# Performance work log

Measured on AMD Instinct MI355X. Metric: run time of the kernel, lower is better.

Reference implementation:

```python
import jax, jax.numpy as jnp
import numpy as np


def _block(x, a, b):
    # [..., W, H, D] -> [..., W//a, H//b, a, b, D]
    w, h, d = x.shape[-3:]
    x = jnp.reshape(x, x.shape[:-3] + (w // a, a, h // b, b, d))
    return jnp.moveaxis(x, -4, -3)


def _combine(x, bs):
    # [..., W, H, D] -> [..., W//bs, H//bs, bs*bs*D]
    x = _block(x, bs, bs)
    return jnp.reshape(x, x.shape[:-3] + (-1,))


def _normalize(x):
    x = x - jnp.mean(x, axis=-1, keepdims=True)
    return x / (jnp.linalg.norm(x, axis=-1, keepdims=True) + 1e-05)


def setup_inputs() -> dict:
    key = jax.random.key(0)
    k1, k2 = jax.random.split(key)
    x = jax.random.normal(k1, (8, 128, 128, 64), dtype=jnp.float32)
    y = jax.random.normal(k2, (8, 128, 128, 64), dtype=jnp.float32)
    return {"x": x, "y": y, "blocksize": 4}


def reference(x, y, blocksize):
    shape = x.shape
    xc = _normalize(_combine(x, blocksize))  # [B, W/bs, H/bs, F]
    yc = _normalize(_combine(y, blocksize))
    yf = jnp.reshape(yc, (-1, yc.shape[-1]))  # [M, F] codebook
    # single similarity matrix, reused for min-loss and argmax (original
    # computed jnp.inner twice -- same math)
    sim = jnp.einsum('...f,mf->...m', xc, yf)  # [B, W/bs, H/bs, M]
    cosloss = jnp.mean(jnp.min(1.0 - sim, axis=-1))
    idx = jnp.argmax(sim, axis=-1)
    # one-hot matmul against yf == top-1 gather (argmax picks first max, as
    # does the original I = (argmax - arange == 0) construction)
    new_x = jnp.take(yf, idx, axis=0)  # [B, W/bs, H/bs, F]
    new_x = jnp.reshape(new_x, new_x.shape[:-1] + (blocksize, blocksize, -1))
    new_x = jnp.swapaxes(new_x, -4, -3)
    new_x = jnp.reshape(new_x, shape)
    return cosloss, new_x
```

## Files before the change

### kernel.cpp

```cpp
#include <hip/hip_runtime.h>
#include <math.h>


#define NROWS 8192
#define KY 1024
#define NCH 32
#define EPS 3e-4f
#define FEPS 8e-4f

typedef _Float16 v8h __attribute__((ext_vector_type(8)));
typedef float f32x4 __attribute__((ext_vector_type(4)));

__device__ __forceinline__ void gload16(const _Float16* g, _Float16* l) {
    __builtin_amdgcn_global_load_lds(
        (const __attribute__((address_space(1))) void*)g,
        (__attribute__((address_space(3))) void*)l, 16, 0, 0);
}

__device__ __forceinline__ unsigned umax(unsigned a, unsigned b) { return a > b ? a : b; }
__device__ __forceinline__ unsigned umin(unsigned a, unsigned b) { return a < b ? a : b; }

__device__ __forceinline__ unsigned packKey(float v, int col) {
    unsigned b = __float_as_uint(v);
    b ^= (unsigned)((int)b >> 31) | 0x80000000u;
    return (b & 0xFFFFE000u) | (unsigned)(8191 - col);
}

__device__ __forceinline__ float unpackApprox(unsigned k) {
    unsigned kb = k & 0xFFFFE000u;
    unsigned b = (kb & 0x80000000u) ? (kb ^ 0x80000000u) : ~kb;
    return __uint_as_float(b);
}

#define KMERGE(a1, a2, a3, b1, b2, b3) do {                                 \
    unsigned _n1 = umax(a1, b1);                                            \
    unsigned _n2 = umax(umin(a1, b1), umax(a2, b2));                        \
    unsigned _n3 = umax(umax(a3, b3), umax(umin(a1, b2), umin(a2, b1)));    \
    a1 = _n1; a2 = _n2; a3 = _n3;                                           \
} while (0)

__global__ __launch_bounds__(256) void normSplitKernel(
    const float* __restrict__ x, const float* __restrict__ y,
    _Float16* __restrict__ Xh, _Float16* __restrict__ Xl,
    _Float16* __restrict__ Yh, _Float16* __restrict__ Yl,
    int* __restrict__ flagCnt) {
    if (blockIdx.x == 0 && threadIdx.x == 0) *flagCnt = 0;
    int gr = blockIdx.x * 4 + (threadIdx.x >> 6);
    int ln = threadIdx.x & 63;
    bool isX = gr < NROWS;
    int row = isX ? gr : gr - NROWS;
    const float* src = isX ? x : y;
    _Float16* dh = isX ? Xh : Yh;
    _Float16* dl = isX ? Xl : Yl;
    int b = row >> 10, wq = (row >> 5) & 31, hq = row & 31;
    int a = ln >> 4, c = (ln >> 2) & 3, d0 = (ln & 3) << 4;
    const float* p = &src[(((size_t)(b * 128) + wq * 4 + a) * 128 + hq * 4 + c) * 64 + d0];
    float vv[16];
    *(float4*)(vv + 0)  = *(const float4*)(p + 0);
    *(float4*)(vv + 4)  = *(const float4*)(p + 4);
    *(float4*)(vv + 8)  = *(const float4*)(p + 8);
    *(float4*)(vv + 12) = *(const float4*)(p + 12);
    double s = 0.0;
    #pragma unroll
    for (int q = 0; q < 16; q++) s += (double)vv[q];
    #pragma unroll
    for (int m = 1; m < 64; m <<= 1) s += __shfl_xor(s, m, 64);
    double mean = s * (1.0 / 1024.0);
    double ss = 0.0;
    #pragma unroll
    for (int q = 0; q < 16; q++) {
        double d = (double)vv[q] - mean;
        ss += d * d;
    }
    #pragma unroll
    for (int m = 1; m < 64; m <<= 1) ss += __shfl_xor(ss, m, 64);
    double scale = 1.0 / (sqrt(ss) + 1e-5);
    _Float16 hi[16], lo[16];
    #pragma unroll
    for (int q = 0; q < 16; q++) {
        float f = (float)(((double)vv[q] - mean) * scale);
        _Float16 h = (_Float16)f;
        hi[q] = h;
        lo[q] = (_Float16)(f - (float)h);
    }
    size_t f0 = (size_t)row * KY + (ln << 4);
    *(v8h*)&dh[f0]     = *(v8h*)(hi);
    *(v8h*)&dh[f0 + 8] = *(v8h*)(hi + 8);
    *(v8h*)&dl[f0]     = *(v8h*)(lo);
    *(v8h*)&dl[f0 + 8] = *(v8h*)(lo + 8);
}

__global__ __launch_bounds__(512, 2) void simKernel(
    const _Float16* __restrict__ Xh, const _Float16* __restrict__ Yh,
    float* __restrict__ pV1, unsigned* __restrict__ pK1,
    unsigned* __restrict__ pK2, unsigned* __restrict__ pK3) {
    __shared__ __align__(16) _Float16 As[2][256 * 64];
    __shared__ __align__(16) _Float16 Bs[2][256 * 64];
    __shared__ unsigned sK[2][4][128][3];
    __shared__ float sE[2][4][128];
    const int t = threadIdx.x;
    const int l = t & 63, w = t >> 6;
    const int wr = w >> 2, wc = w & 3;
    const int quad = l >> 4, lm = l & 15;
    const int flat = blockIdx.x;
    const int bx = flat >> 5, by = flat & 31;
    const int r0 = bx * 256, c0 = by * 256;

    f32x4 acc[8][4];
    #pragma unroll
    for (int i = 0; i < 8; i++)
        #pragma unroll
        for (int j = 0; j < 4; j++) acc[i][j] = (f32x4){0.f, 0.f, 0.f, 0.f};

    const int lh = l >> 3, ll = l & 7;
    const int srow = w * 8 + lh;
    const int scol = (ll ^ lh) << 3;
    const _Float16* gA0 = Xh + (size_t)(r0 + srow) * KY + scol;
    const _Float16* gB0 = Yh + (size_t)(c0 + srow) * KY + scol;
    const int ldsS = w * 512;

#define STAGE(bb, kt) do {                                                   \
    const size_t _ko = (size_t)(kt) * 64;                                    \
    gload16(gA0 + _ko,                       &As[bb][ldsS]);                 \
    gload16(gB0 + _ko,                       &Bs[bb][ldsS]);                 \
    gload16(gA0 + (size_t)64  * KY + _ko,    &As[bb][4096 + ldsS]);          \
    gload16(gB0 + (size_t)64  * KY + _ko,    &Bs[bb][4096 + ldsS]);          \
    gload16(gA0 + (size_t)128 * KY + _ko,    &As[bb][8192 + ldsS]);          \
    gload16(gB0 + (size_t)128 * KY + _ko,    &Bs[bb][8192 + ldsS]);          \
    gload16(gA0 + (size_t)192 * KY + _ko,    &As[bb][12288 + ldsS]);         \
    gload16(gB0 + (size_t)192 * KY + _ko,    &Bs[bb][12288 + ldsS]);         \
} while (0)

    const int arow = (wr * 128 + lm) * 64;
    const int brow = (wc * 64 + lm) * 64;
    const int sw7 = lm & 7;

    STAGE(0, 0);
    asm volatile("s_waitcnt vmcnt(0)" ::: "memory");
    __builtin_amdgcn_s_barrier();
    __builtin_amdgcn_sched_barrier(0);

    #pragma unroll 1
    for (int kt = 0; kt < 16; kt++) {
        const int cur = kt & 1;
        STAGE(cur ^ 1, (kt + 1) & 15);
        #pragma unroll
        for (int ks = 0; ks < 2; ks++) {
            const int cA = ((ks * 4 + quad) ^ sw7) << 3;
            v8h af[8], bf[4];
            #pragma unroll
            for (int i = 0; i < 8; i++)
                af[i] = *(const v8h*)&As[cur][arow + i * 1024 + cA];
            #pragma unroll
            for (int j = 0; j < 4; j++)
                bf[j] = *(const v8h*)&Bs[cur][brow + j * 1024 + cA];
            __builtin_amdgcn_s_setprio(1);
            #pragma unroll
            for (int j = 0; j < 4; j++)
                #pragma unroll
                for (int i = 0; i < 8; i++)
                    acc[i][j] = __builtin_amdgcn_mfma_f32_16x16x32_f16(af[i], bf[j], acc[i][j], 0, 0, 0);
            __builtin_amdgcn_s_setprio(0);
        }
        asm volatile("s_waitcnt vmcnt(0)" ::: "memory");
        __builtin_amdgcn_s_barrier();
        __builtin_amdgcn_sched_barrier(0);
    }
#undef STAGE

    const int cbase = c0 + wc * 64 + lm;
    #pragma unroll
    for (int i = 0; i < 8; i++) {
        #pragma unroll
        for (int r = 0; r < 4; r++) {
            float v0 = acc[i][0][r], v1 = acc[i][1][r];
            float v2 = acc[i][2][r], v3 = acc[i][3][r];
            unsigned k0 = packKey(v0, cbase);
            unsigned k1 = packKey(v1, cbase + 16);
            unsigned k2 = packKey(v2, cbase + 32);
            unsigned k3 = packKey(v3, cbase + 48);
            unsigned h1 = umax(k0, k1), l1 = umin(k0, k1);
            unsigned h2 = umax(k2, k3), l2 = umin(k2, k3);
            unsigned a1 = umax(h1, h2);
            unsigned a2 = umax(umin(h1, h2), umax(l1, l2));
            unsigned a3 = umax(umin(h1, l2), umin(l1, h2));
            float ev = fmaxf(fmaxf(v0, v1), fmaxf(v2, v3));
            #pragma unroll
            for (int m = 1; m < 16; m <<= 1) {
                unsigned b1 = (unsigned)__shfl_xor((int)a1, m, 64);
                unsigned b2 = (unsigned)__shfl_xor((int)a2, m, 64);
                unsigned b3 = (unsigned)__shfl_xor((int)a3, m, 64);
                float be = __shfl_xor(ev, m, 64);
                KMERGE(a1, a2, a3, b1, b2, b3);
                ev = fmaxf(ev, be);
            }
            if (lm == 0) {
                int rr = i * 16 + quad * 4 + r;
                sK[wr][wc][rr][0] = a1; sK[wr][wc][rr][1] = a2; sK[wr][wc][rr][2] = a3;
                sE[wr][wc][rr] = ev;
            }
        }
    }
    __syncthreads();
    if (t < 256) {
        const int mwr = t >> 7, ri = t & 127;
        unsigned a1 = sK[mwr][0][ri][0], a2 = sK[mwr][0][ri][1], a3 = sK[mwr][0][ri][2];
        float ev = sE[mwr][0][ri];
        #pragma unroll
        for (int q = 1; q < 4; q++) {
            unsigned b1 = sK[mwr][q][ri][0], b2 = sK[mwr][q][ri][1], b3 = sK[mwr][q][ri][2];
            KMERGE(a1, a2, a3, b1, b2, b3);
            ev = fmaxf(ev, sE[mwr][q][ri]);
        }
        size_t o = (size_t)by * NROWS + (r0 + t);
        pV1[o] = ev;
        pK1[o] = a1; pK2[o] = a2; pK3[o] = a3;
    }
}

__global__ __launch_bounds__(256) void reduceKernel(
    const float* __restrict__ pV1, const unsigned* __restrict__ pK1,
    const unsigned* __restrict__ pK2, const unsigned* __restrict__ pK3,
    int* __restrict__ bestIdx, int* __restrict__ flagRows,
    int* __restrict__ flagC2, int* __restrict__ flagC3,
    int* __restrict__ flagCnt, float* __restrict__ blkSum) {
    int t = threadIdx.x;
    int g = blockIdx.x * 256 + t;
    int row = g >> 2, sub = g & 3;
    unsigned a1 = 0, a2 = 0, a3 = 0;
    float ev = -1e30f;
    #pragma unroll
    for (int k = 0; k < 8; k++) {
        size_t o = (size_t)(sub + (k << 2)) * NROWS + row;
        unsigned b1 = pK1[o], b2 = pK2[o], b3 = pK3[o];
        float e = pV1[o];
        KMERGE(a1, a2, a3, b1, b2, b3);
        ev = fmaxf(ev, e);
    }
    #pragma unroll
    for (int m = 1; m < 4; m <<= 1) {
        unsigned b1 = (unsigned)__shfl_xor((int)a1, m, 64);
        unsigned b2 = (unsigned)__shfl_xor((int)a2, m, 64);
        unsigned b3 = (unsigned)__shfl_xor((int)a3, m, 64);
        float be = __shfl_xor(ev, m, 64);
        KMERGE(a1, a2, a3, b1, b2, b3);
        ev = fmaxf(ev, be);
    }
    bool lead = (t & 3) == 0;
    if (lead) {
        bestIdx[row] = 8191 - (int)(a1 & 8191u);
        if (ev - unpackApprox(a2) < FEPS) {
            int s = atomicAdd(flagCnt, 1);
            flagRows[s] = row;
            flagC2[s] = 8191 - (int)(a2 & 8191u);
            flagC3[s] = 8191 - (int)(a3 & 8191u);
        }
    }
    double sum = lead ? 1.0 - (double)ev : 0.0;
    __shared__ double sh[4];
    #pragma unroll
    for (int off = 32; off; off >>= 1) sum += __shfl_down(sum, off, 64);
    if ((t & 63) == 0) sh[t >> 6] = sum;
    __syncthreads();
    if (t == 0) blkSum[blockIdx.x] = (float)(sh[0] + sh[1] + sh[2] + sh[3]);
}

__global__ __launch_bounds__(256) void refineKernel(
    const _Float16* __restrict__ Xh, const _Float16* __restrict__ Xl,
    const _Float16* __restrict__ Yh, const _Float16* __restrict__ Yl,
    int* __restrict__ bestIdx, const int* __restrict__ flagRows,
    const int* __restrict__ flagC2, const int* __restrict__ flagC3,
    const int* __restrict__ flagCnt) {
    int n = *flagCnt;
    int wave = (blockIdx.x << 2) + (threadIdx.x >> 6);
    int ln = threadIdx.x & 63;
    for (int fi = wave; fi < n; fi += gridDim.x * 4) {
        int row = flagRows[fi];
        int cand[3];
        cand[0] = bestIdx[row]; cand[1] = flagC2[fi]; cand[2] = flagC3[fi];
        double d[3];
        #pragma unroll
        for (int c = 0; c < 3; c++) {
            double p = 0.0;
            int yr = cand[c];
            #pragma unroll
            for (int q = 0; q < 16; q++) {
                int k = (ln << 4) + q;
                float xv = (float)Xh[(size_t)row * KY + k] + (float)Xl[(size_t)row * KY + k];
                float yv = (float)Yh[(size_t)yr * KY + k] + (float)Yl[(size_t)yr * KY + k];
                p += (double)xv * yv;
            }
            #pragma unroll
            for (int m = 1; m < 64; m <<= 1) p += __shfl_xor(p, m, 64);
            d[c] = p;
        }
        if (ln == 0) {
            int bi = cand[0]; double bv = d[0];
            #pragma unroll
            for (int c = 1; c < 3; c++) {
                if (d[c] > bv || (d[c] == bv && cand[c] < bi)) { bv = d[c]; bi = cand[c]; }
            }
            bestIdx[row] = bi;
        }
    }
}

__global__ __launch_bounds__(256) void gatherKernel(
    const _Float16* __restrict__ Yh, const _Float16* __restrict__ Yl,
    const int* __restrict__ bestIdx, const float* __restrict__ blkSum,
    float* __restrict__ out) {
    int t = threadIdx.x;
    if (blockIdx.x == 0 && t == 0) {
        double s = 0.0;
        for (int i = 0; i < 128; i++) s += (double)blkSum[i];
        out[0] = (float)(s / 8192.0);
    }
    int g = (blockIdx.x * 256 + t) << 2;
    int b = g >> 20, wq = (g >> 13) & 127, hq = (g >> 6) & 127, d = g & 63;
    int row = (b << 10) + ((wq >> 2) << 5) + (hq >> 2);
    int f = ((wq & 3) << 8) + ((hq & 3) << 6) + d;
    size_t base = (size_t)bestIdx[row] * KY + f;
    const _Float16* ph = &Yh[base];
    const _Float16* pl = &Yl[base];
    out[1 + g + 0] = (float)ph[0] + (float)pl[0];
    out[1 + g + 1] = (float)ph[1] + (float)pl[1];
    out[1 + g + 2] = (float)ph[2] + (float)pl[2];
    out[1 + g + 3] = (float)ph[3] + (float)pl[3];
}

extern "C" void kernel_launch(void* const* d_in, const int* in_sizes, int n_in,
                              void* d_out, int out_size, void* d_ws, size_t ws_size,
                              hipStream_t stream) {
    const float* x = (const float*)d_in[0];
    const float* y = (const float*)d_in[1];
    float* out = (float*)d_out;
    char* ws = (char*)d_ws;
    _Float16* Xh  = (_Float16*)(ws);
    _Float16* Xl  = (_Float16*)(ws + 16777216u);
    _Float16* Yh  = (_Float16*)(ws + 33554432u);
    _Float16* Yl  = (_Float16*)(ws + 50331648u);
    float* pV1    = (float*)(ws + 67108864u);
    unsigned* pK1 = (unsigned*)(ws + 69206016u);
    unsigned* pK2 = (unsigned*)(ws + 71303168u);
    unsigned* pK3 = (unsigned*)(ws + 73400320u);
    int* bestIdx  = (int*)  (ws + 79691776u);
    int* flagRows = (int*)  (ws + 79724544u);
    int* flagC2   = (int*)  (ws + 79757312u);
    int* flagC3   = (int*)  (ws + 79790080u);
    int* flagCnt  = (int*)  (ws + 79822848u);
    float* blkSum = (float*)(ws + 79822976u);

    normSplitKernel<<<4096, 256, 0, stream>>>(x, y, Xh, Xl, Yh, Yl, flagCnt);
    simKernel<<<1024, 512, 0, stream>>>(Xh, Yh, pV1, pK1, pK2, pK3);
    reduceKernel<<<128, 256, 0, stream>>>(pV1, pK1, pK2, pK3,
                                          bestIdx, flagRows, flagC2, flagC3, flagCnt, blkSum);
    refineKernel<<<64, 256, 0, stream>>>(Xh, Xl, Yh, Yl, bestIdx,
                                         flagRows, flagC2, flagC3, flagCnt);
    gatherKernel<<<8192, 256, 0, stream>>>(Yh, Yl, bestIdx, blkSum, out);
}
```

Measured before the change: 320.7 us.

## Split GEMM main loop into four interleaved load/MFMA phases with finer barriers

```diff
diff --git a/kernel.cpp b/kernel.cpp
--- a/kernel.cpp
+++ b/kernel.cpp
@@ -94,8 +94,8 @@
     const _Float16* __restrict__ Xh, const _Float16* __restrict__ Yh,
     float* __restrict__ pV1, unsigned* __restrict__ pK1,
     unsigned* __restrict__ pK2, unsigned* __restrict__ pK3) {
-    __shared__ __align__(16) _Float16 As[2][256 * 64];
-    __shared__ __align__(16) _Float16 Bs[2][256 * 64];
+    __shared__ __align__(16) _Float16 As[2][2][128 * 64];
+    __shared__ __align__(16) _Float16 Bs[2][2][128 * 64];
     __shared__ unsigned sK[2][4][128][3];
     __shared__ float sE[2][4][128];
     const int t = threadIdx.x;
@@ -112,61 +112,102 @@
         #pragma unroll
         for (int j = 0; j < 4; j++) acc[i][j] = (f32x4){0.f, 0.f, 0.f, 0.f};
 
-    const int lh = l >> 3, ll = l & 7;
-    const int srow = w * 8 + lh;
-    const int scol = (ll ^ lh) << 3;
-    const _Float16* gA0 = Xh + (size_t)(r0 + srow) * KY + scol;
-    const _Float16* gB0 = Yh + (size_t)(c0 + srow) * KY + scol;
-    const int ldsS = w * 512;
-
-#define STAGE(bb, kt) do {                                                   \
-    const size_t _ko = (size_t)(kt) * 64;                                    \
-    gload16(gA0 + _ko,                       &As[bb][ldsS]);                 \
-    gload16(gB0 + _ko,                       &Bs[bb][ldsS]);                 \
-    gload16(gA0 + (size_t)64  * KY + _ko,    &As[bb][4096 + ldsS]);          \
-    gload16(gB0 + (size_t)64  * KY + _ko,    &Bs[bb][4096 + ldsS]);          \
-    gload16(gA0 + (size_t)128 * KY + _ko,    &As[bb][8192 + ldsS]);          \
-    gload16(gB0 + (size_t)128 * KY + _ko,    &Bs[bb][8192 + ldsS]);          \
-    gload16(gA0 + (size_t)192 * KY + _ko,    &As[bb][12288 + ldsS]);         \
-    gload16(gB0 + (size_t)192 * KY + _ko,    &Bs[bb][12288 + ldsS]);         \
+    const int lh = l >> 3;
+    const int scol = ((l & 7) ^ lh) << 3;
+    const _Float16* gA = Xh + (size_t)(r0 + w * 8 + lh) * KY + scol;
+    const _Float16* gB = Yh + (size_t)(c0 + w * 8 + lh) * KY + scol;
+    const int w512 = w * 512;
+
+#define STAGE_H(Ms, gM, bb, h, ktt) do {                                       \
+    gload16(gM + (size_t)((h) * 128) * KY + (ktt) * 64,      &Ms[bb][h][w512]); \
+    gload16(gM + (size_t)((h) * 128 + 64) * KY + (ktt) * 64, &Ms[bb][h][w512 + 4096]); \
 } while (0)
 
-    const int arow = (wr * 128 + lm) * 64;
-    const int brow = (wc * 64 + lm) * 64;
     const int sw7 = lm & 7;
-
-    STAGE(0, 0);
+    const int cK0 = (quad ^ sw7) << 3;
+    const int cK1 = ((4 + quad) ^ sw7) << 3;
+    const int aOff = lm * 64;
+    const int bSub = (wc & 1) * 4096 + lm * 64;
+
+    STAGE_H(As, gA, 0, 0, 0); STAGE_H(As, gA, 0, 1, 0);
+    STAGE_H(Bs, gB, 0, 0, 0); STAGE_H(Bs, gB, 0, 1, 0);
     asm volatile("s_waitcnt vmcnt(0)" ::: "memory");
     __builtin_amdgcn_s_barrier();
-    __builtin_amdgcn_sched_barrier(0);
 
     #pragma unroll 1
     for (int kt = 0; kt < 16; kt++) {
-        const int cur = kt & 1;
-        STAGE(cur ^ 1, (kt + 1) & 15);
-        #pragma unroll
-        for (int ks = 0; ks < 2; ks++) {
-            const int cA = ((ks * 4 + quad) ^ sw7) << 3;
-            v8h af[8], bf[4];
-            #pragma unroll
-            for (int i = 0; i < 8; i++)
-                af[i] = *(const v8h*)&As[cur][arow + i * 1024 + cA];
-            #pragma unroll
-            for (int j = 0; j < 4; j++)
-                bf[j] = *(const v8h*)&Bs[cur][brow + j * 1024 + cA];
-            __builtin_amdgcn_s_setprio(1);
-            #pragma unroll
-            for (int j = 0; j < 4; j++)
-                #pragma unroll
-                for (int i = 0; i < 8; i++)
-                    acc[i][j] = __builtin_amdgcn_mfma_f32_16x16x32_f16(af[i], bf[j], acc[i][j], 0, 0, 0);
-            __builtin_amdgcn_s_setprio(0);
-        }
+        const int b = kt & 1, bn = b ^ 1;
+        const int ktn = (kt + 1) & 15;
+        const _Float16* Ah = &As[b][wr][0];
+        const _Float16* Bh = &Bs[b][wc >> 1][0];
+        v8h af[4], bf[4];
+
+        #pragma unroll
+        for (int i = 0; i < 4; i++) af[i] = *(const v8h*)&Ah[i * 1024 + aOff + cK0];
+        #pragma unroll
+        for (int j = 0; j < 4; j++) bf[j] = *(const v8h*)&Bh[bSub + j * 1024 + cK0];
+        STAGE_H(As, gA, bn, 0, ktn);
+        __builtin_amdgcn_s_barrier();
+        asm volatile("s_waitcnt lgkmcnt(0)" ::: "memory");
+        __builtin_amdgcn_sched_barrier(0);
+        __builtin_amdgcn_s_setprio(1);
+        #pragma unroll
+        for (int j = 0; j < 4; j++)
+            #pragma unroll
+            for (int i = 0; i < 4; i++)
+                acc[i][j] = __builtin_amdgcn_mfma_f32_16x16x32_f16(af[i], bf[j], acc[i][j], 0, 0, 0);
+        __builtin_amdgcn_s_setprio(0);
+        __builtin_amdgcn_s_barrier();
+
+        #pragma unroll
+        for (int i = 0; i < 4; i++) af[i] = *(const v8h*)&Ah[4096 + i * 1024 + aOff + cK0];
+        STAGE_H(As, gA, bn, 1, ktn);
+        __builtin_amdgcn_s_barrier();
+        asm volatile("s_waitcnt lgkmcnt(0)" ::: "memory");
+        __builtin_amdgcn_sched_barrier(0);
+        __builtin_amdgcn_s_setprio(1);
+        #pragma unroll
+        for (int j = 0; j < 4; j++)
+            #pragma unroll
+            for (int i = 0; i < 4; i++)
+                acc[4 + i][j] = __builtin_amdgcn_mfma_f32_16x16x32_f16(af[i], bf[j], acc[4 + i][j], 0, 0, 0);
+        __builtin_amdgcn_s_setprio(0);
+        __builtin_amdgcn_s_barrier();
+
+        #pragma unroll
+        for (int i = 0; i < 4; i++) af[i] = *(const v8h*)&Ah[i * 1024 + aOff + cK1];
+        #pragma unroll
+        for (int j = 0; j < 4; j++) bf[j] = *(const v8h*)&Bh[bSub + j * 1024 + cK1];
+        STAGE_H(Bs, gB, bn, 0, ktn);
+        __builtin_amdgcn_s_barrier();
+        asm volatile("s_waitcnt lgkmcnt(0)" ::: "memory");
+        __builtin_amdgcn_sched_barrier(0);
+        __builtin_amdgcn_s_setprio(1);
+        #pragma unroll
+        for (int j = 0; j < 4; j++)
+            #pragma unroll
+            for (int i = 0; i < 4; i++)
+                acc[i][j] = __builtin_amdgcn_mfma_f32_16x16x32_f16(af[i], bf[j], acc[i][j], 0, 0, 0);
+        __builtin_amdgcn_s_setprio(0);
+        __builtin_amdgcn_s_barrier();
+
+        #pragma unroll
+        for (int i = 0; i < 4; i++) af[i] = *(const v8h*)&Ah[4096 + i * 1024 + aOff + cK1];
+        STAGE_H(Bs, gB, bn, 1, ktn);
+        __builtin_amdgcn_s_barrier();
+        asm volatile("s_waitcnt lgkmcnt(0)" ::: "memory");
+        __builtin_amdgcn_sched_barrier(0);
+        __builtin_amdgcn_s_setprio(1);
+        #pragma unroll
+        for (int j = 0; j < 4; j++)
+            #pragma unroll
+            for (int i = 0; i < 4; i++)
+                acc[4 + i][j] = __builtin_amdgcn_mfma_f32_16x16x32_f16(af[i], bf[j], acc[4 + i][j], 0, 0, 0);
+        __builtin_amdgcn_s_setprio(0);
         asm volatile("s_waitcnt vmcnt(0)" ::: "memory");
         __builtin_amdgcn_s_barrier();
-        __builtin_amdgcn_sched_barrier(0);
-    }
-#undef STAGE
+    }
+#undef STAGE_H
 
     const int cbase = c0 + wc * 64 + lm;
     #pragma unroll
```

Measured after the change: 320.3 us. Within noise of the previous version (-0.2%).
